# Kernel optimization log

Measured on AMD Instinct MI355X. Metric: run time of the kernel, lower is better.

Reference implementation:

```python
import jax, jax.numpy as jnp
import numpy as np

DIM = 96
SHIFT_SIZE = 3
EPS = 1e-5


def conv1x1(x, w, b):
    # x: [B,C,H,W], w: [O,C], b: [O]
    return jnp.einsum('bchw,oc->bohw', x, w) + b[None, :, None, None]


def group_norm1(x, gamma, beta):
    # GroupNorm with 1 group: normalize over (C,H,W) per sample
    mean = jnp.mean(x, axis=(1, 2, 3), keepdims=True)
    var = jnp.var(x, axis=(1, 2, 3), keepdims=True)
    xn = (x - mean) * jax.lax.rsqrt(var + EPS)
    return xn * gamma[None, :, None, None] + beta[None, :, None, None]


def axial_shift(x, shift_size, axis, sign=1):
    # pad -> chunk channels -> roll each chunk -> cat -> narrow (zero-fill shift)
    B, C, H, W = x.shape
    p = shift_size // 2
    xp = jnp.pad(x, ((0, 0), (0, 0), (p, p), (p, p)))
    chunks = jnp.split(xp, shift_size, axis=1)
    rolled = [jnp.roll(c, sign * s, axis=axis) for c, s in zip(chunks, range(-p, p + 1))]
    xc = jnp.concatenate(rolled, axis=1)
    return xc[:, :, p:p + H, p:p + W]


def setup_inputs() -> dict:
    key = jax.random.key(0)
    ks = jax.random.split(key, 13)
    B, C, H, W = 4, DIM, 256, 256
    s = 1.0 / np.sqrt(C)
    inp = {
        'x': jax.random.normal(ks[0], (B, C, H, W), jnp.float32),
        'w1': jax.random.uniform(ks[1], (C, C), jnp.float32, -s, s),
        'b1': jax.random.uniform(ks[2], (C,), jnp.float32, -s, s),
        'w21': jax.random.uniform(ks[3], (C, C), jnp.float32, -s, s),
        'b21': jax.random.uniform(ks[4], (C,), jnp.float32, -s, s),
        'w22': jax.random.uniform(ks[5], (C, C), jnp.float32, -s, s),
        'b22': jax.random.uniform(ks[6], (C,), jnp.float32, -s, s),
        'w3': jax.random.uniform(ks[7], (C, C), jnp.float32, -s, s),
        'b3': jax.random.uniform(ks[8], (C,), jnp.float32, -s, s),
        'gn1_w': jnp.ones((C,), jnp.float32),
        'gn1_b': jnp.zeros((C,), jnp.float32),
        'gn2_w': jnp.ones((C,), jnp.float32),
        'gn2_b': jnp.zeros((C,), jnp.float32),
    }
    return inp


def reference(x, w1, b1, w21, b21, w22, b22, w3, b3, gn1_w, gn1_b, gn2_w, gn2_b):
    gelu = lambda t: jax.nn.gelu(t, approximate=False)  # torch nn.GELU default (erf)
    x = gelu(group_norm1(conv1x1(x, w1, b1), gn1_w, gn1_b))
    x_lr = axial_shift(x, SHIFT_SIZE, axis=3)
    x_l_diag = axial_shift(x_lr, SHIFT_SIZE, axis=2)
    x_td = axial_shift(x, SHIFT_SIZE, axis=2)
    x_r_diag = axial_shift(x_td, SHIFT_SIZE, axis=3, sign=-1)
    out = (gelu(conv1x1(x_lr, w21, b21)) + gelu(conv1x1(x_l_diag, w21, b21))
           + gelu(conv1x1(x_td, w22, b22)) + gelu(conv1x1(x_r_diag, w22, b22)))
    out = group_norm1(out, gn2_w, gn2_b)
    return conv1x1(out, w3, b3)
```

## Files before the change

kernel.cpp:

```cpp
#include <hip/hip_runtime.h>
#include <hip/hip_bf16.h>
#include <math.h>


#define B_ 4
#define C_ 96
#define H_ 256
#define W_ 256
#define NPIX (H_ * W_)
#define GN_N ((float)(C_ * NPIX))
#define CPAD 104

#define HT 8
#define WT 16
#define HHT (HT + 2)
#define HWT (WT + 2)
#define HALO_PX (HHT * HWT)
#define GR_PX 12
#define ROW_GR (HWT * GR_PX)
#define TOT_GR (HHT * ROW_GR)

typedef __attribute__((ext_vector_type(4))) float f32x4;
typedef __attribute__((ext_vector_type(8))) short short8;
typedef __attribute__((ext_vector_type(2))) unsigned int uint2v;

__device__ __forceinline__ unsigned short f2bf(float v) {
    unsigned int u = __float_as_uint(v);
    unsigned int r = (u + 0x7FFFu + ((u >> 16) & 1u)) >> 16;
    return (unsigned short)r;
}
__device__ __forceinline__ float bf2f(unsigned short u) {
    return __uint_as_float(((unsigned int)u) << 16);
}

__device__ __forceinline__ float gelu_f(float v) {
    float t = fmaf(v * v, 0.1029433f, 2.3021178f);
    float e = __builtin_amdgcn_exp2f(v * t);
    float r = __builtin_amdgcn_rcpf(e + 1.0f);
    return v - v * r;
}

__device__ __forceinline__ float waveReduceSum(float v) {
#pragma unroll
    for (int off = 32; off > 0; off >>= 1) v += __shfl_down(v, off);
    return v;
}

__device__ __forceinline__ f32x4 mfma16(short8 a, short8 b, f32x4 c) {
    return __builtin_amdgcn_mfma_f32_16x16x32_bf16(a, b, c, 0, 0, 0);
}

__global__ void k0_prep(const float* __restrict__ w1, const float* __restrict__ w21,
                        const float* __restrict__ w22, const float* __restrict__ w3,
                        unsigned short* __restrict__ wb, float* __restrict__ stats) {
    int t = blockIdx.x * 256 + threadIdx.x;
    if (blockIdx.x == 0 && threadIdx.x < 16) stats[threadIdx.x] = 0.f;
    if (t >= 4 * C_ * C_) return;
    int m = t / (C_ * C_);
    int r = t - m * (C_ * C_);
    const float* src = (m == 0) ? w1 : (m == 1) ? w21 : (m == 2) ? w22 : w3;
    wb[t] = f2bf(src[r]);
}

__global__ __launch_bounds__(256, 3) void k1_conv1(
    const float* __restrict__ x, const unsigned short* __restrict__ w1b,
    const float* __restrict__ b1, unsigned short* __restrict__ ap,
    float* __restrict__ stats) {
    __shared__ unsigned short xs[256 * CPAD];
    __shared__ float red[8];
    int tid = threadIdx.x;
    int b = blockIdx.x >> 8;
    int h = blockIdx.x & 255;
    int pix0 = h << 8;
    size_t xbase = (size_t)b * C_ * NPIX + pix0 + tid;
    int lb = tid * CPAD;
#pragma unroll
    for (int c0 = 0; c0 < C_; c0 += 8) {
        short8 pk;
#pragma unroll
        for (int j = 0; j < 8; ++j)
            pk[j] = (short)f2bf(x[xbase + (size_t)(c0 + j) * NPIX]);
        *reinterpret_cast<short8*>(&xs[lb + c0]) = pk;
    }
    __syncthreads();
    int l = tid & 63, wv = tid >> 6;
    int bx = l & 15, q = l >> 4, cl = q * 8;
    short8 bfr[4][3];
#pragma unroll
    for (int nf = 0; nf < 4; ++nf) {
        int p = (4 * wv + nf) * 16 + bx;
#pragma unroll
        for (int kb = 0; kb < 3; ++kb)
            bfr[nf][kb] = *reinterpret_cast<const short8*>(&xs[p * CPAD + kb * 32 + cl]);
    }
    unsigned int* xsu = reinterpret_cast<unsigned int*>(xs);
    float ls = 0.f, lsq = 0.f;
    for (int mt = 0; mt < 6; ++mt) {
        int m0 = mt * 16;
        const unsigned short* wp = w1b + (m0 + bx) * C_ + cl;
        short8 af[3];
#pragma unroll
        for (int kb = 0; kb < 3; ++kb)
            af[kb] = *reinterpret_cast<const short8*>(wp + kb * 32);
        f32x4 acc[4];
#pragma unroll
        for (int nf = 0; nf < 4; ++nf) acc[nf] = (f32x4){0.f, 0.f, 0.f, 0.f};
#pragma unroll
        for (int nf = 0; nf < 4; ++nf)
#pragma unroll
            for (int kb = 0; kb < 3; ++kb)
                acc[nf] = mfma16(af[kb], bfr[nf][kb], acc[nf]);
        int o = m0 + q * 4;
        float b0 = b1[o], b1v = b1[o + 1], b2v = b1[o + 2], b3v = b1[o + 3];
#pragma unroll
        for (int nf = 0; nf < 4; ++nf) {
            int p = (4 * wv + nf) * 16 + bx;
            float y0 = acc[nf][0] + b0, y1v = acc[nf][1] + b1v;
            float y2 = acc[nf][2] + b2v, y3 = acc[nf][3] + b3v;
            ls += y0 + y1v + y2 + y3;
            lsq += y0 * y0 + y1v * y1v + y2 * y2 + y3 * y3;
            xsu[p * (CPAD / 2) + (o >> 1)] =
                (unsigned int)f2bf(y0) | ((unsigned int)f2bf(y1v) << 16);
            xsu[p * (CPAD / 2) + (o >> 1) + 1] =
                (unsigned int)f2bf(y2) | ((unsigned int)f2bf(y3) << 16);
        }
    }
    __syncthreads();
    size_t abase = (size_t)(b * NPIX + pix0 + tid) * C_;
#pragma unroll
    for (int c0 = 0; c0 < C_; c0 += 8)
        *reinterpret_cast<short8*>(&ap[abase + c0]) =
            *reinterpret_cast<short8*>(&xs[tid * CPAD + c0]);
    ls = waveReduceSum(ls);
    lsq = waveReduceSum(lsq);
    if (l == 0) { red[wv] = ls; red[4 + wv] = lsq; }
    __syncthreads();
    if (tid == 0) {
        atomicAdd(&stats[b], red[0] + red[1] + red[2] + red[3]);
        atomicAdd(&stats[4 + b], red[4] + red[5] + red[6] + red[7]);
    }
}

__global__ void k2_fin(float* stats, int so, int dof) {
    int t = threadIdx.x;
    if (t < 4) {
        float mean = stats[so + t] / GN_N;
        float var = stats[so + 4 + t] / GN_N - mean * mean;
        stats[dof + t] = mean;
        stats[dof + 4 + t] = rsqrtf(var + 1e-5f);
    }
}

__global__ __launch_bounds__(256, 4) void k3_main(
    const unsigned short* __restrict__ ap,
    const unsigned short* __restrict__ w21b, const float* __restrict__ b21,
    const unsigned short* __restrict__ w22b, const float* __restrict__ b22,
    const float* __restrict__ gn1w, const float* __restrict__ gn1b,
    unsigned short* __restrict__ zb, float* __restrict__ stats) {
    __shared__ unsigned short as_t[HALO_PX * CPAD];
    __shared__ float red[8];
    __shared__ float scs[C_], offs[C_];
    int tid = threadIdx.x;
    int wseg = blockIdx.x & 15;
    int hseg = (blockIdx.x >> 4) & 31;
    int b = blockIdx.x >> 9;
    int l = tid & 63, wv = tid >> 6;
    int h0 = hseg * HT, w0 = wseg * WT;
    float m1 = stats[16 + b], r1 = stats[20 + b];
    if (tid < C_) {
        float sc = r1 * gn1w[tid];
        scs[tid] = sc;
        offs[tid] = gn1b[tid] - m1 * sc;
    }
    __syncthreads();
    for (int g = tid; g < TOT_GR; g += 256) {
        int row = g / ROW_GR;
        int rem = g - row * ROW_GR;
        int p = rem / GR_PX;
        int cgr = rem - p * GR_PX;
        int hh = h0 - 1 + row, ww = w0 - 1 + p;
        bool valid = ((unsigned)hh < (unsigned)H_) && ((unsigned)ww < (unsigned)W_);
        int hc = valid ? hh : 0, wc = valid ? ww : 0;
        short8 raw = *reinterpret_cast<const short8*>(
            &ap[(size_t)(b * NPIX + hc * W_ + wc) * C_ + cgr * 8]);
        short8 pk;
#pragma unroll
        for (int j = 0; j < 8; ++j) {
            int c = cgr * 8 + j;
            float f = bf2f((unsigned short)raw[j]);
            float gv = gelu_f(fmaf(f, scs[c], offs[c]));
            pk[j] = valid ? (short)f2bf(gv) : (short)0;
        }
        *reinterpret_cast<short8*>(&as_t[(row * HWT + p) * CPAD + cgr * 8]) = pk;
    }
    __syncthreads();
    int bx = l & 15, q = l >> 4, cl = q * 8;
    int Xb = (bx + 1) * CPAD + cl;
#define FR(R, dx, kb) (*reinterpret_cast<const short8*>( \
        &as_t[((R)*HWT + (dx)) * CPAD + Xb + (kb)*32]))
    float ls = 0.f, lsq = 0.f;
#pragma unroll
    for (int nf = 0; nf < 2; ++nf) {
        int r = 2 * wv + nf;
        short8 f0a = FR(r + 1, 1, 0), f0b = FR(r + 2, 1, 0);
        short8 f0c = FR(r + 2, 0, 0), f0d = FR(r + 2, -1, 0);
        short8 fC = FR(r + 1, 0, 1);
        short8 f2a = FR(r + 1, -1, 2), f2b = FR(r, -1, 2);
        short8 f2c = FR(r, 0, 2), f2d = FR(r, 1, 2);
        size_t zpix = (size_t)(b * NPIX + (h0 + r) * W_ + w0 + bx) * C_;
        for (int mt = 0; mt < 6; ++mt) {
            int m0 = mt * 16;
            const unsigned short* wpa = w21b + (m0 + bx) * C_ + cl;
            const unsigned short* wpb = w22b + (m0 + bx) * C_ + cl;
            short8 aA0 = *reinterpret_cast<const short8*>(wpa);
            short8 aA1 = *reinterpret_cast<const short8*>(wpa + 32);
            short8 aA2 = *reinterpret_cast<const short8*>(wpa + 64);
            short8 aB0 = *reinterpret_cast<const short8*>(wpb);
            short8 aB1 = *reinterpret_cast<const short8*>(wpb + 32);
            short8 aB2 = *reinterpret_cast<const short8*>(wpb + 64);
            const f32x4 bb1 = *reinterpret_cast<const f32x4*>(&b21[m0 + q * 4]);
            const f32x4 bb2 = *reinterpret_cast<const f32x4*>(&b22[m0 + q * 4]);
            f32x4 a0 = bb1, a1 = bb1, a2 = bb2, a3 = bb2;
            a0 = mfma16(aA0, f0a, a0);
            a1 = mfma16(aA0, f0b, a1);
            a2 = mfma16(aB0, f0c, a2);
            a3 = mfma16(aB0, f0d, a3);
            a0 = mfma16(aA1, fC, a0);
            a1 = mfma16(aA1, fC, a1);
            a2 = mfma16(aB1, fC, a2);
            a3 = mfma16(aB1, fC, a3);
            a0 = mfma16(aA2, f2a, a0);
            a1 = mfma16(aA2, f2b, a1);
            a2 = mfma16(aB2, f2c, a2);
            a3 = mfma16(aB2, f2d, a3);
            float zv[4];
#pragma unroll
            for (int rg = 0; rg < 4; ++rg) {
                float z0 = gelu_f(a0[rg]) + gelu_f(a1[rg]) +
                           gelu_f(a2[rg]) + gelu_f(a3[rg]);
                zv[rg] = z0;
                ls += z0;
                lsq += z0 * z0;
            }
            uint2v pk;
            pk.x = (unsigned int)f2bf(zv[0]) | ((unsigned int)f2bf(zv[1]) << 16);
            pk.y = (unsigned int)f2bf(zv[2]) | ((unsigned int)f2bf(zv[3]) << 16);
            *reinterpret_cast<uint2v*>(&zb[zpix + m0 + q * 4]) = pk;
        }
    }
#undef FR
    ls = waveReduceSum(ls);
    lsq = waveReduceSum(lsq);
    if (l == 0) { red[wv] = ls; red[4 + wv] = lsq; }
    __syncthreads();
    if (tid == 0) {
        atomicAdd(&stats[8 + b], red[0] + red[1] + red[2] + red[3]);
        atomicAdd(&stats[12 + b], red[4] + red[5] + red[6] + red[7]);
    }
}

__global__ void k4b_fold(const float* __restrict__ w3, const float* __restrict__ b3,
                         const float* __restrict__ gn2w, const float* __restrict__ gn2b,
                         const float* __restrict__ stats,
                         unsigned short* __restrict__ w3p, float* __restrict__ b3p) {
    int b = blockIdx.x;
    int o = threadIdx.x;
    float mean = stats[8 + b] / GN_N;
    float var = stats[12 + b] / GN_N - mean * mean;
    float r2 = rsqrtf(var + 1e-5f);
    float acc = 0.f;
    for (int c = 0; c < C_; ++c) {
        float sc = r2 * gn2w[c];
        float off = gn2b[c] - mean * sc;
        float wv = w3[o * C_ + c];
        acc = fmaf(wv, off, acc);
        w3p[((size_t)b * C_ + o) * C_ + c] = f2bf(wv * sc);
    }
    b3p[b * C_ + o] = acc + b3[o];
}

__global__ __launch_bounds__(256, 3) void k5_conv3(
    const unsigned short* __restrict__ zb,
    const unsigned short* __restrict__ w3p, const float* __restrict__ b3p,
    float* __restrict__ out) {
    __shared__ unsigned short zs[256 * CPAD];
    int tid = threadIdx.x;
    int b = blockIdx.x >> 8;
    int pix0 = (blockIdx.x & 255) << 8;
    {
        const short8* src = reinterpret_cast<const short8*>(
            &zb[(size_t)(b * NPIX + pix0 + tid) * C_]);
        int lb = tid * CPAD;
#pragma unroll
        for (int i = 0; i < 12; ++i)
            *reinterpret_cast<short8*>(&zs[lb + i * 8]) = src[i];
    }
    __syncthreads();
    int l = tid & 63, wv = tid >> 6;
    int bx = l & 15, q = l >> 4, cl = q * 8;
    short8 bfr[4][3];
#pragma unroll
    for (int nf = 0; nf < 4; ++nf) {
        int p = (4 * wv + nf) * 16 + bx;
#pragma unroll
        for (int kb = 0; kb < 3; ++kb)
            bfr[nf][kb] = *reinterpret_cast<const short8*>(&zs[p * CPAD + kb * 32 + cl]);
    }
    const unsigned short* wbase = w3p + (size_t)b * C_ * C_;
    const float* bb = b3p + b * C_;
    for (int mt = 0; mt < 6; ++mt) {
        int m0 = mt * 16;
        const unsigned short* wp = wbase + (m0 + bx) * C_ + cl;
        short8 af0 = *reinterpret_cast<const short8*>(wp);
        short8 af1 = *reinterpret_cast<const short8*>(wp + 32);
        short8 af2 = *reinterpret_cast<const short8*>(wp + 64);
        f32x4 acc[4];
#pragma unroll
        for (int nf = 0; nf < 4; ++nf) acc[nf] = (f32x4){0.f, 0.f, 0.f, 0.f};
#pragma unroll
        for (int nf = 0; nf < 4; ++nf) {
            acc[nf] = mfma16(af0, bfr[nf][0], acc[nf]);
            acc[nf] = mfma16(af1, bfr[nf][1], acc[nf]);
            acc[nf] = mfma16(af2, bfr[nf][2], acc[nf]);
        }
        int o = m0 + q * 4;
        float b0 = bb[o], b1v = bb[o + 1], b2v = bb[o + 2], b3v = bb[o + 3];
#pragma unroll
        for (int nf = 0; nf < 4; ++nf) {
            int p = pix0 + (4 * wv + nf) * 16 + bx;
            size_t ob0 = (size_t)(b * C_ + o) * NPIX + p;
            out[ob0] = acc[nf][0] + b0;
            out[ob0 + NPIX] = acc[nf][1] + b1v;
            out[ob0 + 2 * NPIX] = acc[nf][2] + b2v;
            out[ob0 + 3 * NPIX] = acc[nf][3] + b3v;
        }
    }
}

extern "C" void kernel_launch(void* const* d_in, const int* in_sizes, int n_in,
                              void* d_out, int out_size, void* d_ws, size_t ws_size,
                              hipStream_t stream) {
    const float* x = (const float*)d_in[0];
    const float* w1 = (const float*)d_in[1];
    const float* b1 = (const float*)d_in[2];
    const float* w21 = (const float*)d_in[3];
    const float* b21 = (const float*)d_in[4];
    const float* w22 = (const float*)d_in[5];
    const float* b22 = (const float*)d_in[6];
    const float* w3 = (const float*)d_in[7];
    const float* b3 = (const float*)d_in[8];
    const float* gn1w = (const float*)d_in[9];
    const float* gn1b = (const float*)d_in[10];
    const float* gn2w = (const float*)d_in[11];
    const float* gn2b = (const float*)d_in[12];
    float* out = (float*)d_out;
    char* ws = (char*)d_ws;

    const size_t NB = (size_t)B_ * NPIX * C_ * sizeof(unsigned short);
    unsigned short* ap = (unsigned short*)ws;
    unsigned short* zb = (unsigned short*)(ws + NB);
    float* stats = (float*)(ws + 2 * NB);
    unsigned short* wb = (unsigned short*)(ws + 2 * NB + 128);
    unsigned short* w1b = wb;
    unsigned short* w21b = wb + C_ * C_;
    unsigned short* w22b = wb + 2 * C_ * C_;
    unsigned short* w3p = wb + 4 * C_ * C_;
    float* b3p = (float*)(w3p + B_ * C_ * C_);

    hipLaunchKernelGGL(k0_prep, dim3(144), dim3(256), 0, stream,
                       w1, w21, w22, w3, wb, stats);
    hipLaunchKernelGGL(k1_conv1, dim3(1024), dim3(256), 0, stream, x, w1b, b1, ap, stats);
    hipLaunchKernelGGL(k2_fin, dim3(1), dim3(64), 0, stream, stats, 0, 16);
    hipLaunchKernelGGL(k3_main, dim3(2048), dim3(256), 0, stream,
                       ap, w21b, b21, w22b, b22, gn1w, gn1b, zb, stats);
    hipLaunchKernelGGL(k4b_fold, dim3(B_), dim3(C_), 0, stream,
                       w3, b3, gn2w, gn2b, stats, w3p, b3p);
    hipLaunchKernelGGL(k5_conv3, dim3(1024), dim3(256), 0, stream,
                       zb, w3p, b3p, out);
}
```

Before: 176.2 us.

## Use hardware bf16 pack conversion and double k3 block to 512 threads

Replaces the software round-to-nearest bf16 packing with the v_cvt_pk_bf16_f32 instruction in k1 and k3. k3_main now runs 512 threads per block, with each wave handling one output row instead of two, so more waves share the halo tile already staged in LDS. The halo fill skips the global load and GELU for out-of-bounds pixels, and the reduction buffer grows to hold eight waves. The larger blocks may limit occupancy through registers or LDS, and the halo fill is now amortised over half the per-wave work.

```diff
diff --git a/kernel.cpp b/kernel.cpp
--- a/kernel.cpp
+++ b/kernel.cpp
@@ -23,14 +23,20 @@
 typedef __attribute__((ext_vector_type(4))) float f32x4;
 typedef __attribute__((ext_vector_type(8))) short short8;
 typedef __attribute__((ext_vector_type(2))) unsigned int uint2v;
-
+typedef __attribute__((ext_vector_type(4))) unsigned int uint4v;
+
+__device__ __forceinline__ float bf2f(unsigned short u) {
+    return __uint_as_float(((unsigned int)u) << 16);
+}
 __device__ __forceinline__ unsigned short f2bf(float v) {
     unsigned int u = __float_as_uint(v);
     unsigned int r = (u + 0x7FFFu + ((u >> 16) & 1u)) >> 16;
     return (unsigned short)r;
 }
-__device__ __forceinline__ float bf2f(unsigned short u) {
-    return __uint_as_float(((unsigned int)u) << 16);
+__device__ __forceinline__ unsigned int cvtpk(float lo, float hi) {
+    unsigned int r;
+    asm("v_cvt_pk_bf16_f32 %0, %1, %2" : "=v"(r) : "v"(lo), "v"(hi));
+    return r;
 }
 
 __device__ __forceinline__ float gelu_f(float v) {
@@ -76,11 +82,12 @@
     int lb = tid * CPAD;
 #pragma unroll
     for (int c0 = 0; c0 < C_; c0 += 8) {
-        short8 pk;
-#pragma unroll
-        for (int j = 0; j < 8; ++j)
-            pk[j] = (short)f2bf(x[xbase + (size_t)(c0 + j) * NPIX]);
-        *reinterpret_cast<short8*>(&xs[lb + c0]) = pk;
+        float f[8];
+#pragma unroll
+        for (int j = 0; j < 8; ++j) f[j] = x[xbase + (size_t)(c0 + j) * NPIX];
+        uint4v pk = {cvtpk(f[0], f[1]), cvtpk(f[2], f[3]),
+                     cvtpk(f[4], f[5]), cvtpk(f[6], f[7])};
+        *reinterpret_cast<uint4v*>(&xs[lb + c0]) = pk;
     }
     __syncthreads();
     int l = tid & 63, wv = tid >> 6;
@@ -119,10 +126,8 @@
             float y2 = acc[nf][2] + b2v, y3 = acc[nf][3] + b3v;
             ls += y0 + y1v + y2 + y3;
             lsq += y0 * y0 + y1v * y1v + y2 * y2 + y3 * y3;
-            xsu[p * (CPAD / 2) + (o >> 1)] =
-                (unsigned int)f2bf(y0) | ((unsigned int)f2bf(y1v) << 16);
-            xsu[p * (CPAD / 2) + (o >> 1) + 1] =
-                (unsigned int)f2bf(y2) | ((unsigned int)f2bf(y3) << 16);
+            xsu[p * (CPAD / 2) + (o >> 1)] = cvtpk(y0, y1v);
+            xsu[p * (CPAD / 2) + (o >> 1) + 1] = cvtpk(y2, y3);
         }
     }
     __syncthreads();
@@ -151,14 +156,14 @@
     }
 }
 
-__global__ __launch_bounds__(256, 4) void k3_main(
+__global__ __launch_bounds__(512, 6) void k3_main(
     const unsigned short* __restrict__ ap,
     const unsigned short* __restrict__ w21b, const float* __restrict__ b21,
     const unsigned short* __restrict__ w22b, const float* __restrict__ b22,
     const float* __restrict__ gn1w, const float* __restrict__ gn1b,
     unsigned short* __restrict__ zb, float* __restrict__ stats) {
     __shared__ unsigned short as_t[HALO_PX * CPAD];
-    __shared__ float red[8];
+    __shared__ float red[16];
     __shared__ float scs[C_], offs[C_];
     int tid = threadIdx.x;
     int wseg = blockIdx.x & 15;
@@ -173,25 +178,28 @@
         offs[tid] = gn1b[tid] - m1 * sc;
     }
     __syncthreads();
-    for (int g = tid; g < TOT_GR; g += 256) {
+    for (int g = tid; g < TOT_GR; g += 512) {
         int row = g / ROW_GR;
         int rem = g - row * ROW_GR;
         int p = rem / GR_PX;
         int cgr = rem - p * GR_PX;
         int hh = h0 - 1 + row, ww = w0 - 1 + p;
-        bool valid = ((unsigned)hh < (unsigned)H_) && ((unsigned)ww < (unsigned)W_);
-        int hc = valid ? hh : 0, wc = valid ? ww : 0;
-        short8 raw = *reinterpret_cast<const short8*>(
-            &ap[(size_t)(b * NPIX + hc * W_ + wc) * C_ + cgr * 8]);
-        short8 pk;
-#pragma unroll
-        for (int j = 0; j < 8; ++j) {
-            int c = cgr * 8 + j;
-            float f = bf2f((unsigned short)raw[j]);
-            float gv = gelu_f(fmaf(f, scs[c], offs[c]));
-            pk[j] = valid ? (short)f2bf(gv) : (short)0;
-        }
-        *reinterpret_cast<short8*>(&as_t[(row * HWT + p) * CPAD + cgr * 8]) = pk;
+        unsigned short* dst = &as_t[(row * HWT + p) * CPAD + cgr * 8];
+        if (((unsigned)hh < (unsigned)H_) && ((unsigned)ww < (unsigned)W_)) {
+            short8 raw = *reinterpret_cast<const short8*>(
+                &ap[(size_t)(b * NPIX + hh * W_ + ww) * C_ + cgr * 8]);
+            float gv[8];
+#pragma unroll
+            for (int j = 0; j < 8; ++j) {
+                int c = cgr * 8 + j;
+                gv[j] = gelu_f(fmaf(bf2f((unsigned short)raw[j]), scs[c], offs[c]));
+            }
+            uint4v pk = {cvtpk(gv[0], gv[1]), cvtpk(gv[2], gv[3]),
+                         cvtpk(gv[4], gv[5]), cvtpk(gv[6], gv[7])};
+            *reinterpret_cast<uint4v*>(dst) = pk;
+        } else {
+            *reinterpret_cast<uint4v*>(dst) = (uint4v){0, 0, 0, 0};
+        }
     }
     __syncthreads();
     int bx = l & 15, q = l >> 4, cl = q * 8;
@@ -199,9 +207,8 @@
 #define FR(R, dx, kb) (*reinterpret_cast<const short8*>( \
         &as_t[((R)*HWT + (dx)) * CPAD + Xb + (kb)*32]))
     float ls = 0.f, lsq = 0.f;
-#pragma unroll
-    for (int nf = 0; nf < 2; ++nf) {
-        int r = 2 * wv + nf;
+    {
+        int r = wv;
         short8 f0a = FR(r + 1, 1, 0), f0b = FR(r + 2, 1, 0);
         short8 f0c = FR(r + 2, 0, 0), f0d = FR(r + 2, -1, 0);
         short8 fC = FR(r + 1, 0, 1);
@@ -243,19 +250,22 @@
                 lsq += z0 * z0;
             }
             uint2v pk;
-            pk.x = (unsigned int)f2bf(zv[0]) | ((unsigned int)f2bf(zv[1]) << 16);
-            pk.y = (unsigned int)f2bf(zv[2]) | ((unsigned int)f2bf(zv[3]) << 16);
+            pk.x = cvtpk(zv[0], zv[1]);
+            pk.y = cvtpk(zv[2], zv[3]);
             *reinterpret_cast<uint2v*>(&zb[zpix + m0 + q * 4]) = pk;
         }
     }
 #undef FR
     ls = waveReduceSum(ls);
     lsq = waveReduceSum(lsq);
-    if (l == 0) { red[wv] = ls; red[4 + wv] = lsq; }
+    if (l == 0) { red[wv] = ls; red[8 + wv] = lsq; }
     __syncthreads();
     if (tid == 0) {
-        atomicAdd(&stats[8 + b], red[0] + red[1] + red[2] + red[3]);
-        atomicAdd(&stats[12 + b], red[4] + red[5] + red[6] + red[7]);
+        float s0 = 0.f, s1 = 0.f;
+#pragma unroll
+        for (int i = 0; i < 8; ++i) { s0 += red[i]; s1 += red[8 + i]; }
+        atomicAdd(&stats[8 + b], s0);
+        atomicAdd(&stats[12 + b], s1);
     }
 }
 
@@ -371,7 +381,7 @@
                        w1, w21, w22, w3, wb, stats);
     hipLaunchKernelGGL(k1_conv1, dim3(1024), dim3(256), 0, stream, x, w1b, b1, ap, stats);
     hipLaunchKernelGGL(k2_fin, dim3(1), dim3(64), 0, stream, stats, 0, 16);
-    hipLaunchKernelGGL(k3_main, dim3(2048), dim3(256), 0, stream,
+    hipLaunchKernelGGL(k3_main, dim3(2048), dim3(512), 0, stream,
                        ap, w21b, b21, w22b, b22, gn1w, gn1b, zb, stats);
     hipLaunchKernelGGL(k4b_fold, dim3(B_), dim3(C_), 0, stream,
                        w3, b3, gn2w, gn2b, stats, w3p, b3p);
```

Result: no change. 176.7 us (+0.3%).
